# Optimization experiments

Hardware: AMD Instinct MI355X
Metric: run time of the kernel (lower is better)

## Reference

```python
import jax, jax.numpy as jnp
import numpy as np

N = 200000   # 10000 graphs x 20 nodes, stacked
E = 3200000  # avg degree 16
F_IN = 4
H = 32
BN_EPS = 1e-5


def setup_inputs() -> dict:
    key = jax.random.key(0)
    ks = jax.random.split(key, 16)
    s = 0.1
    return {
        "x": jax.random.normal(ks[0], (N, F_IN), jnp.float32),
        "edge_index": jax.random.randint(ks[1], (2, E), 0, N, jnp.int64),
        "edge_weight": jax.random.uniform(ks[2], (E,), jnp.float32),
        "gcn1_w": jax.random.normal(ks[3], (F_IN, H), jnp.float32) * s,
        "gcn1_b": jnp.zeros((H,), jnp.float32),
        "gcn2_w": jax.random.normal(ks[4], (H, H), jnp.float32) * s,
        "gcn2_b": jnp.zeros((H,), jnp.float32),
        "bn1_gamma": jnp.ones((H,), jnp.float32),
        "bn1_beta": jnp.zeros((H,), jnp.float32),
        "bn1_mean": jnp.zeros((H,), jnp.float32),
        "bn1_var": jnp.ones((H,), jnp.float32),
        "bn2_gamma": jnp.ones((H,), jnp.float32),
        "bn2_beta": jnp.zeros((H,), jnp.float32),
        "bn2_mean": jnp.zeros((H,), jnp.float32),
        "bn2_var": jnp.ones((H,), jnp.float32),
        "lstm1_wih": jax.random.normal(ks[5], (4 * H, 2 * H), jnp.float32) * s,
        "lstm1_whh": jax.random.normal(ks[6], (4 * H, H), jnp.float32) * s,
        "lstm1_bih": jax.random.normal(ks[7], (4 * H,), jnp.float32) * s,
        "lstm1_bhh": jax.random.normal(ks[8], (4 * H,), jnp.float32) * s,
        "lstm2_wih": jax.random.normal(ks[9], (4 * H, H), jnp.float32) * s,
        "lstm2_whh": jax.random.normal(ks[10], (4 * H, H), jnp.float32) * s,
        "lstm2_bih": jax.random.normal(ks[11], (4 * H,), jnp.float32) * s,
        "lstm2_bhh": jax.random.normal(ks[12], (4 * H,), jnp.float32) * s,
        "lin_w": jax.random.normal(ks[13], (1, 2 * H + F_IN), jnp.float32) * s,
        "lin_b": jnp.zeros((1,), jnp.float32),
    }


def _gcn_conv(x, src, dst, ew, W, b, n):
    # GCNConv: x @ W, add self-loops (weight 1), symmetric normalization, scatter-add at dst.
    xw = x @ W
    loop = jnp.arange(n)
    s = jnp.concatenate([src, loop])
    d = jnp.concatenate([dst, loop])
    w = jnp.concatenate([ew, jnp.ones((n,), ew.dtype)])
    deg = jax.ops.segment_sum(w, d, num_segments=n)
    dinv = jnp.where(deg > 0, jax.lax.rsqrt(deg), 0.0)
    norm = dinv[s] * w * dinv[d]  # [E+N]
    out = jax.ops.segment_sum(norm[:, None] * xw[s], d, num_segments=n)
    return out + b


def _bn_eval(x, gamma, beta, mean, var):
    return (x - mean) * jax.lax.rsqrt(var + BN_EPS) * gamma + beta


def _lstm_step(x, wih, bih, bhh):
    # single timestep, zero initial (h, c): recurrent W_hh term vanishes.
    gates = x @ wih.T + bih + bhh
    i, f, g, o = jnp.split(gates, 4, axis=1)  # torch gate order i,f,g,o
    c = jax.nn.sigmoid(i) * jnp.tanh(g)
    return jax.nn.sigmoid(o) * jnp.tanh(c)


def reference(x, edge_index, edge_weight, gcn1_w, gcn1_b, gcn2_w, gcn2_b,
              bn1_gamma, bn1_beta, bn1_mean, bn1_var,
              bn2_gamma, bn2_beta, bn2_mean, bn2_var,
              lstm1_wih, lstm1_whh, lstm1_bih, lstm1_bhh,
              lstm2_wih, lstm2_whh, lstm2_bih, lstm2_bhh,
              lin_w, lin_b):
    n = x.shape[0]
    src, dst = edge_index[0], edge_index[1]
    # MPNNLSTM (window=1, eval mode: dropout=identity, BN uses running stats)
    h1 = _bn_eval(jax.nn.relu(_gcn_conv(x, src, dst, edge_weight, gcn1_w, gcn1_b, n)),
                  bn1_gamma, bn1_beta, bn1_mean, bn1_var)
    h2 = _bn_eval(jax.nn.relu(_gcn_conv(h1, src, dst, edge_weight, gcn2_w, gcn2_b, n)),
                  bn2_gamma, bn2_beta, bn2_mean, bn2_var)
    skip = jnp.concatenate([h1, h2], axis=1)  # [N, 2H]
    H1 = _lstm_step(skip, lstm1_wih, lstm1_bih, lstm1_bhh)  # [N, H]
    H2 = _lstm_step(H1, lstm2_wih, lstm2_bih, lstm2_bhh)    # [N, H]
    h = jnp.concatenate([H1, H2, x], axis=1)  # [N, 2H + F_IN]
    # RecurrentGCN head: relu + linear -> [N, 1]
    return jax.nn.relu(h) @ lin_w.T + lin_b
```

## Files before the change

### kernel.cpp

```cpp
#include <hip/hip_runtime.h>
#include <hip/hip_fp16.h>
#include <math.h>

#define BN_EPS 1e-5f
#define HF 32
#define BS 256
#define KEDGE 4096
#define MAXNB 800
#define WQ14 16383.0f
#define WQ22 4194303.0f

typedef _Float16 half8 __attribute__((ext_vector_type(8)));
typedef float f32x4 __attribute__((ext_vector_type(4)));
typedef float f32x2 __attribute__((ext_vector_type(2)));

__device__ __forceinline__ float fsig(float x) {
    return __builtin_amdgcn_rcpf(1.0f + __expf(-x));
}
__device__ __forceinline__ float ftanh(float x) {
    return 1.0f - 2.0f * __builtin_amdgcn_rcpf(1.0f + __expf(2.0f * x));
}


__device__ __forceinline__ float e4m3_to_f32_sw(unsigned v) {
    unsigned s = v & 0x80u, E = (v >> 3) & 0xFu, m = v & 7u;
    float r = E ? ldexpf((float)(8 + m), (int)E - 10) : ldexpf((float)m, -9);
    return s ? -r : r;
}

__device__ __forceinline__ unsigned f32_to_e4m3_sw(float x) {
    float ax = fabsf(x);
    unsigned s = x < 0.0f ? 0x80u : 0u;
    if (!(ax > 0.0f)) return s;
    if (ax >= 448.0f) return s | 0x7Eu;
    int e;
    float m = frexpf(ax, &e);
    int E = e - 1 + 7;
    if (E >= 1) {
        int q = (int)(m * 16.0f + 0.5f);
        if (q == 16) { q = 8; E += 1; if (E > 15) return s | 0x7Eu; }
        return s | (unsigned)(E << 3) | (unsigned)(q - 8);
    }
    int q = (int)(ax * 512.0f + 0.5f);
    if (q > 7) return s | 0x08u;
    return s | (unsigned)q;
}

__device__ __forceinline__ void dec8(uint2 r, float* f) {
#if __has_builtin(__builtin_amdgcn_cvt_pk_f32_fp8)
    f32x2 p0 = __builtin_amdgcn_cvt_pk_f32_fp8((int)r.x, false);
    f32x2 p1 = __builtin_amdgcn_cvt_pk_f32_fp8((int)r.x, true);
    f32x2 p2 = __builtin_amdgcn_cvt_pk_f32_fp8((int)r.y, false);
    f32x2 p3 = __builtin_amdgcn_cvt_pk_f32_fp8((int)r.y, true);
    f[0] = p0[0]; f[1] = p0[1]; f[2] = p1[0]; f[3] = p1[1];
    f[4] = p2[0]; f[5] = p2[1]; f[6] = p3[0]; f[7] = p3[1];
#else
#pragma unroll
    for (int k = 0; k < 4; ++k) f[k] = e4m3_to_f32_sw((r.x >> (8 * k)) & 0xFFu);
#pragma unroll
    for (int k = 0; k < 4; ++k) f[4 + k] = e4m3_to_f32_sw((r.y >> (8 * k)) & 0xFFu);
#endif
}

__device__ __forceinline__ uint2 enc8(const float* o) {
#if __has_builtin(__builtin_amdgcn_cvt_pk_fp8_f32)
    int w0 = 0, w1 = 0;
    w0 = __builtin_amdgcn_cvt_pk_fp8_f32(o[0], o[1], w0, false);
    w0 = __builtin_amdgcn_cvt_pk_fp8_f32(o[2], o[3], w0, true);
    w1 = __builtin_amdgcn_cvt_pk_fp8_f32(o[4], o[5], w1, false);
    w1 = __builtin_amdgcn_cvt_pk_fp8_f32(o[6], o[7], w1, true);
    return make_uint2((unsigned)w0, (unsigned)w1);
#else
    unsigned a = 0, b = 0;
#pragma unroll
    for (int k = 0; k < 4; ++k) a |= f32_to_e4m3_sw(o[k]) << (8 * k);
#pragma unroll
    for (int k = 0; k < 4; ++k) b |= f32_to_e4m3_sw(o[4 + k]) << (8 * k);
    return make_uint2(a, b);
#endif
}


__global__ __launch_bounds__(512) void k_binsort(
        const int* __restrict__ src, const int* __restrict__ dst,
        const float* __restrict__ ew, int E, int NB, int bcap,
        int* __restrict__ gcur, uint2* __restrict__ recs) {
    __shared__ int hist[MAXNB], curs[MAXNB];

    int tid = threadIdx.x;
    int base = blockIdx.x * KEDGE;
    int cnt = min(KEDGE, E - base);

    for (int i = tid; i < NB; i += 512) hist[i] = 0;
    __syncthreads();

    uint2 rec[KEDGE / 512];
#pragma unroll
    for (int k = 0; k < KEDGE / 512; ++k) {
        int i = tid + k * 512;
        if (i < cnt) {
            int s = src[base + i];
            int d = dst[base + i];
            float w = ew[base + i];
            unsigned q = (unsigned)(w * WQ22 + 0.5f);
            if (q > 4194303u) q = 4194303u;
            int b = d >> 8;
            rec[k] = make_uint2(((unsigned)s << 8) | (unsigned)(d & 255),
                                ((unsigned)b << 22) | q);
            atomicAdd(&hist[b], 1);
        }
    }
    __syncthreads();

    for (int b = tid; b < NB; b += 512) {
        int len = hist[b];
        curs[b] = len ? atomicAdd(&gcur[b], len) : 0;
    }
    __syncthreads();

#pragma unroll
    for (int k = 0; k < KEDGE / 512; ++k) {
        int i = tid + k * 512;
        if (i < cnt) {
            uint2 u = rec[k];
            int b = u.y >> 22;
            int off = atomicAdd(&curs[b], 1);
            if (off < bcap) recs[(size_t)b * bcap + off] = u;
        }
    }
}


__global__ __launch_bounds__(512) void k_sortb(
        const uint2* __restrict__ recs, const int* __restrict__ gcur,
        int bcap, int bcap4,
        const float* __restrict__ x, const float* __restrict__ W1,
        unsigned* __restrict__ recs4, int* __restrict__ pstart,
        int* __restrict__ pcnt, float* __restrict__ dinv,
        unsigned char* __restrict__ y18, int n) {
    __shared__ int hist[BS], excl4[BS], curs[BS], wsm[BS];
    __shared__ float sdv[BS];
    __shared__ float sW1[128];

    int b = blockIdx.x, tid = threadIdx.x;
    int cnt = min(gcur[b], bcap);
    const uint2* r = recs + (size_t)b * bcap;
    const float dq = 1.0f / WQ22;

    if (tid < BS) { hist[tid] = 0; wsm[tid] = 0; }
    if (tid >= 256 && tid < 384) sW1[tid - 256] = W1[tid - 256];
    __syncthreads();

    for (int i = tid; i < cnt; i += 512) {
        uint2 u = r[i];
        int dl = u.x & 255;
        atomicAdd(&hist[dl], 1);
        atomicAdd(&wsm[dl], (int)(u.y & 4194303u));
    }
    __syncthreads();

    if (tid < BS) {
        int g = b * BS + tid;
        sdv[tid] = (g < n) ? rsqrtf(1.0f + (float)wsm[tid] * dq) : 0.0f;
    }
    if (tid < 64) {
        int run = 0;
        for (int c = 0; c < BS; c += 64) {
            int idx = c + tid;
            int v = (hist[idx] + 3) & ~3;
            int incl = v;
#pragma unroll
            for (int o = 1; o < 64; o <<= 1) {
                int up = __shfl_up(incl, o, 64);
                if (tid >= o) incl += up;
            }
            int e = run + incl - v;
            excl4[idx] = e; curs[idx] = e;
            run += __shfl(incl, 63, 64);
        }
    }
    __syncthreads();

    unsigned* out4 = recs4 + (size_t)b * bcap4;
    for (int i = tid; i < cnt; i += 512) {
        uint2 u = r[i];
        int dl = u.x & 255;
        int pos = atomicAdd(&curs[dl], 1);
        float qn = (float)(u.y & 4194303u) * dq * sdv[dl];
        unsigned q = (unsigned)(qn * WQ14 + 0.5f);
        if (q > 16383u) q = 16383u;
        out4[pos] = ((u.x >> 8) << 14) | q;
    }

    {
        int node = tid >> 1, half = tid & 1;
        int g = b * BS + node;
        if (g < n) {
            float4 xv = *(const float4*)(x + (size_t)g * 4);
            float sc = sdv[node];
            int f0 = half * 16;
            float o[16];
#pragma unroll
            for (int k = 0; k < 16; ++k)
                o[k] = sc * (xv.x * sW1[f0 + k] + xv.y * sW1[32 + f0 + k] +
                             xv.z * sW1[64 + f0 + k] + xv.w * sW1[96 + f0 + k]);
            uint2 lo = enc8(o), hi = enc8(o + 8);
            *(uint4*)(y18 + ((size_t)g << 5) + half * 16) = make_uint4(lo.x, lo.y, hi.x, hi.y);
        }
    }

    if (tid < BS) {
        int g = b * BS + tid;
        if (g < n) {
            pstart[g] = b * bcap4 + excl4[tid];
            pcnt[g] = hist[tid];
            dinv[g] = sdv[tid];
        }
    }
}


__global__ __launch_bounds__(256) void k_prep(
        const float* __restrict__ wih1, const float* __restrict__ bih1,
        const float* __restrict__ bhh1, const float* __restrict__ wih2,
        const float* __restrict__ bih2, const float* __restrict__ bhh2,
        __half* __restrict__ wp1, __half* __restrict__ wp2,
        float* __restrict__ bsum1, float* __restrict__ bsum2,
        int* __restrict__ gcur, int NB) {
    const int tg[6] = {0, 16, 64, 80, 96, 112};
    int idx = blockIdx.x * 256 + threadIdx.x;
    if (idx < 6144) {
        int t = idx >> 10, rem = idx & 1023;
        int kc = rem >> 9, rem2 = rem & 511;
        int lane = rem2 >> 3, j = rem2 & 7;
        int g = tg[t] + (lane & 15);
        int k = kc * 32 + (lane >> 4) * 8 + j;
        wp1[idx] = __float2half(wih1[g * 64 + k]);
    } else if (idx < 9216) {
        int i2 = idx - 6144;
        int t = i2 >> 9, rem2 = i2 & 511;
        int lane = rem2 >> 3, j = rem2 & 7;
        int g = tg[t] + (lane & 15);
        int k = (lane >> 4) * 8 + j;
        wp2[i2] = __float2half(wih2[g * 32 + k]);
    } else if (idx < 9344) {
        int i = idx - 9216;
        bsum1[i] = bih1[i] + bhh1[i];
    } else if (idx < 9472) {
        int i = idx - 9344;
        bsum2[i] = bih2[i] + bhh2[i];
    } else if (idx < 9472 + NB) {
        gcur[idx - 9472] = 0;
    }
}


__global__ __launch_bounds__(256) void k_g1w2(
        const unsigned* __restrict__ recs4, const int* __restrict__ pstart,
        const int* __restrict__ pcnt, const float* __restrict__ dinv,
        const unsigned char* __restrict__ y18, const float* __restrict__ W2,
        const float* __restrict__ bias, const float* __restrict__ gamma,
        const float* __restrict__ beta, const float* __restrict__ mean,
        const float* __restrict__ var,
        __half* __restrict__ skiph, unsigned char* __restrict__ A8, int n) {
    __shared__ float sW2[1024];
    __shared__ float sh1[64][33];
    int tid = threadIdx.x;
    for (int i = tid; i < 1024; i += 256) sW2[i] = W2[i];
    __syncthreads();

    int nl = tid >> 2;
    int g = blockIdx.x * 64 + nl;
    int lane = tid & 3;
    int fq = lane * 8;
    bool act = g < n;

    float acc[8];
#pragma unroll
    for (int k = 0; k < 8; ++k) acc[k] = 0.0f;

    float dig = 0.0f;
    if (act) {
        dig = dinv[g];
        {
            uint2 sr = ((const uint2*)(y18 + ((size_t)g << 5)))[lane];
            float f[8];
            dec8(sr, f);
#pragma unroll
            for (int k = 0; k < 8; ++k) acc[k] = dig * f[k];
        }

        const float qs = 1.0f / WQ14;
        int cn = pcnt[g];
        const unsigned* r = recs4 + pstart[g];
        int e = 0;
        for (; e + 8 <= cn; e += 8) {
            uint4 ua = *(const uint4*)(r + e);
            uint4 ub = *(const uint4*)(r + e + 4);
            unsigned u[8] = {ua.x, ua.y, ua.z, ua.w, ub.x, ub.y, ub.z, ub.w};
            uint2 rw[8];
#pragma unroll
            for (int q = 0; q < 8; ++q)
                rw[q] = ((const uint2*)(y18 + ((size_t)(u[q] >> 14) << 5)))[lane];
            float nm[8];
#pragma unroll
            for (int q = 0; q < 8; ++q)
                nm[q] = (float)(u[q] & 16383u) * qs;
#pragma unroll
            for (int q = 0; q < 8; ++q) {
                float f[8];
                dec8(rw[q], f);
#pragma unroll
                for (int k = 0; k < 8; ++k) acc[k] += nm[q] * f[k];
            }
        }
        for (; e < cn; ++e) {
            unsigned u0 = r[e];
            uint2 r0 = ((const uint2*)(y18 + ((size_t)(u0 >> 14) << 5)))[lane];
            float n0 = (float)(u0 & 16383u) * qs;
            float f[8];
            dec8(r0, f);
#pragma unroll
            for (int k = 0; k < 8; ++k) acc[k] += n0 * f[k];
        }
    }

    float o[8];
#pragma unroll
    for (int k = 0; k < 8; ++k) {
        float v = fmaxf(acc[k] + bias[fq + k], 0.0f);
        o[k] = (v - mean[fq + k]) * gamma[fq + k] * rsqrtf(var[fq + k] + BN_EPS) + beta[fq + k];
        sh1[nl][fq + k] = o[k];
    }
    if (act) {
        union { __half h[8]; uint4 q; } hv;
#pragma unroll
        for (int k = 0; k < 8; ++k) hv.h[k] = __float2half(o[k]);
        *(uint4*)(skiph + (size_t)g * 64 + fq) = hv.q;
    }
    __syncthreads();

    if (act) {
        float a2[8];
#pragma unroll
        for (int j = 0; j < 8; ++j) a2[j] = 0.0f;
#pragma unroll 4
        for (int k = 0; k < 32; ++k) {
            float h = sh1[nl][k];
            const float* wr = sW2 + k * 32 + fq;
#pragma unroll
            for (int j = 0; j < 8; ++j) a2[j] += h * wr[j];
        }
#pragma unroll
        for (int j = 0; j < 8; ++j) a2[j] *= dig;
        ((uint2*)(A8 + ((size_t)g << 5)))[lane] = enc8(a2);
    }
}


__global__ __launch_bounds__(256) void k_gather8(
        const unsigned* __restrict__ recs4, const int* __restrict__ pstart,
        const int* __restrict__ pcnt, const float* __restrict__ dinv,
        const unsigned char* __restrict__ A8,
        const float* __restrict__ bias, const float* __restrict__ gamma,
        const float* __restrict__ beta, const float* __restrict__ mean,
        const float* __restrict__ var,
        __half* __restrict__ skiph, int uoff, int n) {
    int g = blockIdx.x * 64 + (threadIdx.x >> 2);
    int lane = threadIdx.x & 3;
    if (g >= n) return;

    float dig = dinv[g];
    float acc[8];
    {
        uint2 sr = ((const uint2*)(A8 + ((size_t)g << 5)))[lane];
        float f[8];
        dec8(sr, f);
#pragma unroll
        for (int k = 0; k < 8; ++k) acc[k] = dig * f[k];
    }

    const float qs = 1.0f / WQ14;
    int cn = pcnt[g];
    const unsigned* r = recs4 + pstart[g];
    int e = 0;
    for (; e + 8 <= cn; e += 8) {
        uint4 ua = *(const uint4*)(r + e);
        uint4 ub = *(const uint4*)(r + e + 4);
        unsigned u[8] = {ua.x, ua.y, ua.z, ua.w, ub.x, ub.y, ub.z, ub.w};
        uint2 rw[8];
#pragma unroll
        for (int q = 0; q < 8; ++q)
            rw[q] = ((const uint2*)(A8 + ((size_t)(u[q] >> 14) << 5)))[lane];
        float nm[8];
#pragma unroll
        for (int q = 0; q < 8; ++q)
            nm[q] = (float)(u[q] & 16383u) * qs;
#pragma unroll
        for (int q = 0; q < 8; ++q) {
            float f[8];
            dec8(rw[q], f);
#pragma unroll
            for (int k = 0; k < 8; ++k) acc[k] += nm[q] * f[k];
        }
    }
    for (; e < cn; ++e) {
        unsigned u0 = r[e];
        uint2 r0 = ((const uint2*)(A8 + ((size_t)(u0 >> 14) << 5)))[lane];
        float n0 = (float)(u0 & 16383u) * qs;
        float f0[8];
        dec8(r0, f0);
#pragma unroll
        for (int k = 0; k < 8; ++k) acc[k] += n0 * f0[k];
    }

    int fq = lane * 8;
    union { __half h[8]; uint4 q; } hv;
#pragma unroll
    for (int k = 0; k < 8; ++k) {
        float v = fmaxf(acc[k] + bias[fq + k], 0.0f);
        hv.h[k] = __float2half((v - mean[fq + k]) * gamma[fq + k] * rsqrtf(var[fq + k] + BN_EPS) + beta[fq + k]);
    }
    *(uint4*)(skiph + (size_t)g * 64 + uoff + fq) = hv.q;
}


__global__ __launch_bounds__(256) void k_headm(
        const __half* __restrict__ skiph, const float* __restrict__ x,
        const __half* __restrict__ wp1, const __half* __restrict__ wp2,
        const float* __restrict__ bsum1, const float* __restrict__ bsum2,
        const float* __restrict__ lw, const float* __restrict__ lb,
        float* __restrict__ out, int n) {
    __shared__ __align__(16) __half H1lds[4 * 16 * 40];
    int tid = threadIdx.x;
    int w = tid >> 6, l = tid & 63;
    int quad = l >> 4, c = l & 15;
    int node_base = blockIdx.x * 64 + w * 16;

    int arow = node_base + c; if (arow > n - 1) arow = n - 1;
    const half8* ap = (const half8*)(skiph + (size_t)arow * 64);
    half8 a0 = ap[quad];
    half8 a1 = ap[4 + quad];

    const half8* b1 = (const half8*)wp1;
    f32x4 d[6];
#pragma unroll
    for (int t = 0; t < 6; ++t) {
        f32x4 acc = {0.0f, 0.0f, 0.0f, 0.0f};
        acc = __builtin_amdgcn_mfma_f32_16x16x32_f16(a0, b1[(t * 2 + 0) * 64 + l], acc, 0, 0, 0);
        acc = __builtin_amdgcn_mfma_f32_16x16x32_f16(a1, b1[(t * 2 + 1) * 64 + l], acc, 0, 0, 0);
        d[t] = acc;
    }

    float bi0 = bsum1[c],      bi1 = bsum1[16 + c];
    float bg0 = bsum1[64 + c], bg1 = bsum1[80 + c];
    float bo0 = bsum1[96 + c], bo1 = bsum1[112 + c];
    float lwc0 = lw[c], lwc1 = lw[c + 16];

    float pa[4];
#pragma unroll
    for (int r = 0; r < 4; ++r) {
        float cc0 = fsig(d[0][r] + bi0) * ftanh(d[2][r] + bg0);
        float h0 = fsig(d[4][r] + bo0) * ftanh(cc0);
        float cc1 = fsig(d[1][r] + bi1) * ftanh(d[3][r] + bg1);
        float h1 = fsig(d[5][r] + bo1) * ftanh(cc1);
        pa[r] = fmaxf(h0, 0.0f) * lwc0 + fmaxf(h1, 0.0f) * lwc1;
        __half* hp = H1lds + (w * 16 + quad * 4 + r) * 40;
        hp[c] = __float2half(h0);
        hp[c + 16] = __float2half(h1);
    }
    __syncthreads();

    half8 a2 = *(const half8*)(H1lds + (w * 16 + c) * 40 + quad * 8);

    const half8* b2 = (const half8*)wp2;
    f32x4 e[6];
#pragma unroll
    for (int t = 0; t < 6; ++t) {
        f32x4 acc = {0.0f, 0.0f, 0.0f, 0.0f};
        e[t] = __builtin_amdgcn_mfma_f32_16x16x32_f16(a2, b2[t * 64 + l], acc, 0, 0, 0);
    }

    float ci0 = bsum2[c],      ci1 = bsum2[16 + c];
    float cg0 = bsum2[64 + c], cg1 = bsum2[80 + c];
    float co0 = bsum2[96 + c], co1 = bsum2[112 + c];
    float lw2c0 = lw[32 + c], lw2c1 = lw[48 + c];
#pragma unroll
    for (int r = 0; r < 4; ++r) {
        float cc0 = fsig(e[0][r] + ci0) * ftanh(e[2][r] + cg0);
        float h0 = fsig(e[4][r] + co0) * ftanh(cc0);
        float cc1 = fsig(e[1][r] + ci1) * ftanh(e[3][r] + cg1);
        float h1 = fsig(e[5][r] + co1) * ftanh(cc1);
        pa[r] += fmaxf(h0, 0.0f) * lw2c0 + fmaxf(h1, 0.0f) * lw2c1;
    }

#pragma unroll
    for (int m = 1; m < 16; m <<= 1) {
#pragma unroll
        for (int r = 0; r < 4; ++r) pa[r] += __shfl_xor(pa[r], m, 64);
    }

    if (c < 4) {
        int node = node_base + quad * 4 + c;
        if (node < n) {
            const float4 xv = *(const float4*)(x + (size_t)node * 4);
            out[node] = pa[c] + lb[0]
                + fmaxf(xv.x, 0.0f) * lw[64] + fmaxf(xv.y, 0.0f) * lw[65]
                + fmaxf(xv.z, 0.0f) * lw[66] + fmaxf(xv.w, 0.0f) * lw[67];
        }
    }
}


__global__ void k_initdeg(float* __restrict__ deg, int n) {
    int i = blockIdx.x * blockDim.x + threadIdx.x;
    if (i < n) deg[i] = 1.0f;
}

__global__ void k_deg_only(const int* __restrict__ dst, const float* __restrict__ ew,
                           float* __restrict__ deg, int E) {
    int e = blockIdx.x * blockDim.x + threadIdx.x;
    if (e < E) atomicAdd(&deg[dst[e]], ew[e]);
}

__global__ void k_dinv_f(float* __restrict__ deg, int n) {
    int i = blockIdx.x * blockDim.x + threadIdx.x;
    if (i < n) {
        float d = deg[i];
        deg[i] = d > 0.0f ? rsqrtf(d) : 0.0f;
    }
}

__global__ void k_xw1_f(const float* __restrict__ x, const float* __restrict__ W,
                        float* __restrict__ out, int n) {
    int idx = blockIdx.x * blockDim.x + threadIdx.x;
    if (idx >= n * HF) return;
    int nn = idx >> 5, f = idx & 31;
    const float4 xr = *(const float4*)(x + (size_t)nn * 4);
    out[idx] = xr.x * W[f] + xr.y * W[32 + f] + xr.z * W[64 + f] + xr.w * W[96 + f];
}

__global__ void k_xw2_f(const float* __restrict__ Hin, const float* __restrict__ W,
                        float* __restrict__ out, int n) {
    __shared__ float sW[32 * 32];
    __shared__ float sH[8][32];
    int tid = threadIdx.x;
    for (int i = tid; i < 1024; i += 256) sW[i] = W[i];
    int r = tid >> 5, f = tid & 31;
    int nn = blockIdx.x * 8 + r;
    if (nn < n) sH[r][f] = Hin[(size_t)nn * HF + f];
    __syncthreads();
    if (nn >= n) return;
    float acc = 0.0f;
#pragma unroll
    for (int k = 0; k < 32; ++k) acc += sH[r][k] * sW[k * 32 + f];
    out[(size_t)nn * HF + f] = acc;
}

__global__ void k_selfloop(const float* __restrict__ A, const float* __restrict__ dinv,
                           float* __restrict__ B, int n) {
    int idx = blockIdx.x * blockDim.x + threadIdx.x;
    if (idx >= n * HF) return;
    int nn = idx >> 5;
    float di = dinv[nn];
    B[idx] = di * di * A[idx];
}

__global__ void k_scatter(const int* __restrict__ src, const int* __restrict__ dst,
                          const float* __restrict__ ew, const float* __restrict__ dinv,
                          const float* __restrict__ A, float* __restrict__ B, int total) {
    int idx = blockIdx.x * blockDim.x + threadIdx.x;
    if (idx >= total) return;
    int e = idx >> 5, f = idx & 31;
    int s = src[e], d = dst[e];
    float norm = dinv[s] * ew[e] * dinv[d];
    atomicAdd(&B[d * HF + f], norm * A[s * HF + f]);
}

__global__ void k_post(const float* __restrict__ B, const float* __restrict__ bias,
                       const float* __restrict__ gamma, const float* __restrict__ beta,
                       const float* __restrict__ mean, const float* __restrict__ var,
                       float* __restrict__ Hout, int n) {
    int idx = blockIdx.x * blockDim.x + threadIdx.x;
    if (idx >= n * HF) return;
    int f = idx & 31;
    float v = fmaxf(B[idx] + bias[f], 0.0f);
    float sc = gamma[f] * rsqrtf(var[f] + BN_EPS);
    Hout[idx] = (v - mean[f]) * sc + beta[f];
}

__global__ __launch_bounds__(256) void k_head(
        const float* __restrict__ h1, const float* __restrict__ h2,
        const float* __restrict__ x,
        const float* __restrict__ wih1, const float* __restrict__ bih1, const float* __restrict__ bhh1,
        const float* __restrict__ wih2, const float* __restrict__ bih2, const float* __restrict__ bhh2,
        const float* __restrict__ lw, const float* __restrict__ lb,
        float* __restrict__ out, int n) {
    __shared__ float sH1[32 * 256];
    int tid = threadIdx.x;
    int nn = blockIdx.x * 256 + tid;
    if (nn >= n) return;

    const float4* a = (const float4*)(h1 + (size_t)nn * HF);
    const float4* b = (const float4*)(h2 + (size_t)nn * HF);
    float skip[64];
#pragma unroll
    for (int q = 0; q < 8; ++q) {
        float4 v = a[q];
        skip[4 * q] = v.x; skip[4 * q + 1] = v.y; skip[4 * q + 2] = v.z; skip[4 * q + 3] = v.w;
        float4 u = b[q];
        skip[32 + 4 * q] = u.x; skip[33 + 4 * q] = u.y; skip[34 + 4 * q] = u.z; skip[35 + 4 * q] = u.w;
    }

    float oa = lb[0];
#pragma unroll 1
    for (int j = 0; j < 32; ++j) {
        const float4* wi = (const float4*)(wih1 + (size_t)j * 64);
        const float4* wg = (const float4*)(wih1 + (size_t)(64 + j) * 64);
        const float4* wo = (const float4*)(wih1 + (size_t)(96 + j) * 64);
        float gi = bih1[j] + bhh1[j];
        float gg = bih1[64 + j] + bhh1[64 + j];
        float go = bih1[96 + j] + bhh1[96 + j];
#pragma unroll
        for (int q = 0; q < 16; ++q) {
            float4 aa = wi[q], bb = wg[q], cc4 = wo[q];
            float s0 = skip[4 * q], s1 = skip[4 * q + 1], s2 = skip[4 * q + 2], s3 = skip[4 * q + 3];
            gi += aa.x * s0 + aa.y * s1 + aa.z * s2 + aa.w * s3;
            gg += bb.x * s0 + bb.y * s1 + bb.z * s2 + bb.w * s3;
            go += cc4.x * s0 + cc4.y * s1 + cc4.z * s2 + cc4.w * s3;
        }
        float cc = fsig(gi) * ftanh(gg);
        float hh = fsig(go) * ftanh(cc);
        sH1[j * 256 + tid] = hh;
        oa += fmaxf(hh, 0.0f) * lw[j];
    }

#pragma unroll 1
    for (int j = 0; j < 32; ++j) {
        const float4* wi = (const float4*)(wih2 + (size_t)j * 32);
        const float4* wg = (const float4*)(wih2 + (size_t)(64 + j) * 32);
        const float4* wo = (const float4*)(wih2 + (size_t)(96 + j) * 32);
        float gi = bih2[j] + bhh2[j];
        float gg = bih2[64 + j] + bhh2[64 + j];
        float go = bih2[96 + j] + bhh2[96 + j];
#pragma unroll
        for (int q = 0; q < 8; ++q) {
            float4 aa = wi[q], bb = wg[q], cc4 = wo[q];
            float s0 = sH1[(4 * q) * 256 + tid], s1 = sH1[(4 * q + 1) * 256 + tid];
            float s2 = sH1[(4 * q + 2) * 256 + tid], s3 = sH1[(4 * q + 3) * 256 + tid];
            gi += aa.x * s0 + aa.y * s1 + aa.z * s2 + aa.w * s3;
            gg += bb.x * s0 + bb.y * s1 + bb.z * s2 + bb.w * s3;
            go += cc4.x * s0 + cc4.y * s1 + cc4.z * s2 + cc4.w * s3;
        }
        float cc = fsig(gi) * ftanh(gg);
        float hh = fsig(go) * ftanh(cc);
        oa += fmaxf(hh, 0.0f) * lw[32 + j];
    }

    const float4 xv = *(const float4*)(x + (size_t)nn * 4);
    oa += fmaxf(xv.x, 0.0f) * lw[64] + fmaxf(xv.y, 0.0f) * lw[65] +
          fmaxf(xv.z, 0.0f) * lw[66] + fmaxf(xv.w, 0.0f) * lw[67];
    out[nn] = oa;
}


extern "C" void kernel_launch(void* const* d_in, const int* in_sizes, int n_in,
                              void* d_out, int out_size, void* d_ws, size_t ws_size,
                              hipStream_t stream) {
    const float* x   = (const float*)d_in[0];
    const int*   ei  = (const int*)d_in[1];
    const float* ew  = (const float*)d_in[2];
    const float* g1w = (const float*)d_in[3];
    const float* g1b = (const float*)d_in[4];
    const float* g2w = (const float*)d_in[5];
    const float* g2b = (const float*)d_in[6];
    const float* bn1g = (const float*)d_in[7];
    const float* bn1b = (const float*)d_in[8];
    const float* bn1m = (const float*)d_in[9];
    const float* bn1v = (const float*)d_in[10];
    const float* bn2g = (const float*)d_in[11];
    const float* bn2b = (const float*)d_in[12];
    const float* bn2m = (const float*)d_in[13];
    const float* bn2v = (const float*)d_in[14];
    const float* w1ih = (const float*)d_in[15];
    const float* b1ih = (const float*)d_in[17];
    const float* b1hh = (const float*)d_in[18];
    const float* w2ih = (const float*)d_in[19];
    const float* b2ih = (const float*)d_in[21];
    const float* b2hh = (const float*)d_in[22];
    const float* lw   = (const float*)d_in[23];
    const float* lb   = (const float*)d_in[24];
    float* out = (float*)d_out;

    const int N = in_sizes[0] / 4;
    const int E = in_sizes[2];
    const int* src = ei;
    const int* dst = ei + E;

    const int T = 256;
    const int NB = (N + BS - 1) / BS;
    long long meanb = ((long long)BS * E) / (N > 0 ? N : 1);
    int bcap = (int)(meanb + meanb / 4 + 128);
    bcap = (bcap + 3) & ~3;
    int bcap4 = bcap + 3 * BS;

    char* p = (char*)d_ws;
    auto alloc = [&](size_t bytes) { char* q = p; p += (bytes + 255) & ~(size_t)255; return q; };
    int*      gcur   = (int*)alloc(sizeof(int) * NB);
    uint2*    recs   = (uint2*)alloc(sizeof(uint2) * (size_t)NB * bcap);
    unsigned* recs4  = (unsigned*)alloc(sizeof(unsigned) * (size_t)NB * bcap4);
    float*    dinv   = (float*)alloc(sizeof(float) * N);
    int*      pstart = (int*)alloc(sizeof(int) * N);
    int*      pcnt   = (int*)alloc(sizeof(int) * N);
    unsigned char* y18 = (unsigned char*)alloc((size_t)N * HF);
    unsigned char* A8  = (unsigned char*)alloc((size_t)N * HF);
    __half*   skiph  = (__half*)alloc(sizeof(__half) * (size_t)N * 64);
    __half*   wp1    = (__half*)alloc(sizeof(__half) * 6144);
    __half*   wp2    = (__half*)alloc(sizeof(__half) * 3072);
    float*    bsum1  = (float*)alloc(sizeof(float) * 128);
    float*    bsum2  = (float*)alloc(sizeof(float) * 128);
    size_t need = (size_t)(p - (char*)d_ws);

    int bN  = (N + T - 1) / T;
    int bE  = (E + T - 1) / T;
    int bNF = (N * HF + T - 1) / T;
    int bN8 = (N + 7) / 8;
    int bG  = (N + 63) / 64;
    int bBin = (E + KEDGE - 1) / KEDGE;
    int bPrep = (9472 + NB + 255) / 256;

    if (ws_size >= need && NB <= MAXNB && N <= (1 << 18)) {
        k_prep<<<bPrep, 256, 0, stream>>>(w1ih, b1ih, b1hh, w2ih, b2ih, b2hh,
                                          wp1, wp2, bsum1, bsum2, gcur, NB);
        k_binsort<<<bBin, 512, 0, stream>>>(src, dst, ew, E, NB, bcap, gcur, recs);
        k_sortb<<<NB, 512, 0, stream>>>(recs, gcur, bcap, bcap4, x, g1w,
                                        recs4, pstart, pcnt, dinv, y18, N);

        k_g1w2<<<bG, T, 0, stream>>>(recs4, pstart, pcnt, dinv, y18, g2w,
                                     g1b, bn1g, bn1b, bn1m, bn1v, skiph, A8, N);
        k_gather8<<<bG, T, 0, stream>>>(recs4, pstart, pcnt, dinv, A8,
                                        g2b, bn2g, bn2b, bn2m, bn2v, skiph, 32, N);
        k_headm<<<bG, T, 0, stream>>>(skiph, x, wp1, wp2, bsum1, bsum2,
                                      lw, lb, out, N);
    } else {
        size_t Npad = ((size_t)N + 255) & ~(size_t)255;
        float* fdinv = (float*)d_ws;
        float* fA = fdinv + Npad;
        float* fB = fA + (size_t)N * HF;
        float* fC = fB + (size_t)N * HF;
        int bEF = (int)(((long long)E * HF + T - 1) / T);
        int bH = (N + 255) / 256;

        k_initdeg<<<bN, T, 0, stream>>>(fdinv, N);
        k_deg_only<<<bE, T, 0, stream>>>(dst, ew, fdinv, E);
        k_dinv_f<<<bN, T, 0, stream>>>(fdinv, N);

        k_xw1_f<<<bNF, T, 0, stream>>>(x, g1w, fA, N);
        k_selfloop<<<bNF, T, 0, stream>>>(fA, fdinv, fB, N);
        k_scatter<<<bEF, T, 0, stream>>>(src, dst, ew, fdinv, fA, fB, E * HF);
        k_post<<<bNF, T, 0, stream>>>(fB, g1b, bn1g, bn1b, bn1m, bn1v, fC, N);

        k_xw2_f<<<bN8, T, 0, stream>>>(fC, g2w, fA, N);
        k_selfloop<<<bNF, T, 0, stream>>>(fA, fdinv, fB, N);
        k_scatter<<<bEF, T, 0, stream>>>(src, dst, ew, fdinv, fA, fB, E * HF);
        k_post<<<bNF, T, 0, stream>>>(fB, g2b, bn2g, bn2b, bn2m, bn2v, fB, N);

        k_head<<<bH, T, 0, stream>>>(fC, fB, x, w1ih, b1ih, b1hh, w2ih, b2ih, b2hh,
                                     lw, lb, out, N);
    }
}
```

Before: 296.9 us.

## Fuse second GCN gather into LSTM head, vectorize binsort loads, prefetch edge records

The second GCN aggregation kernel is merged into the LSTM/linear head kernel. The h2 features now stay in shared memory instead of going through global memory, so skiph shrinks to only h1 (32 halves per node). Binsort now has each thread load 8 contiguous edges with 128-bit vector loads instead of strided scalar loads. The gather loops software-prefetch the next 8 edge records. The fused kernel uses more shared memory and registers, which may lower occupancy for the latency-bound gather.

```diff
diff --git a/kernel.cpp b/kernel.cpp
--- a/kernel.cpp
+++ b/kernel.cpp
@@ -94,20 +94,42 @@
     for (int i = tid; i < NB; i += 512) hist[i] = 0;
     __syncthreads();
 
-    uint2 rec[KEDGE / 512];
-#pragma unroll
-    for (int k = 0; k < KEDGE / 512; ++k) {
-        int i = tid + k * 512;
-        if (i < cnt) {
-            int s = src[base + i];
-            int d = dst[base + i];
-            float w = ew[base + i];
-            unsigned q = (unsigned)(w * WQ22 + 0.5f);
-            if (q > 4194303u) q = 4194303u;
-            int b = d >> 8;
-            rec[k] = make_uint2(((unsigned)s << 8) | (unsigned)(d & 255),
-                                ((unsigned)b << 22) | q);
-            atomicAdd(&hist[b], 1);
+    uint2 rec[8];
+    int nmine = 0;
+    int eb = base + tid * 8;
+    if (tid * 8 < cnt) {
+        nmine = min(8, cnt - tid * 8);
+        if (nmine == 8) {
+            int4 s0 = *(const int4*)(src + eb);
+            int4 s1 = *(const int4*)(src + eb + 4);
+            int4 d0 = *(const int4*)(dst + eb);
+            int4 d1 = *(const int4*)(dst + eb + 4);
+            float4 w0 = *(const float4*)(ew + eb);
+            float4 w1 = *(const float4*)(ew + eb + 4);
+            int ss[8] = {s0.x, s0.y, s0.z, s0.w, s1.x, s1.y, s1.z, s1.w};
+            int dd[8] = {d0.x, d0.y, d0.z, d0.w, d1.x, d1.y, d1.z, d1.w};
+            float ww[8] = {w0.x, w0.y, w0.z, w0.w, w1.x, w1.y, w1.z, w1.w};
+#pragma unroll
+            for (int k = 0; k < 8; ++k) {
+                unsigned q = (unsigned)(ww[k] * WQ22 + 0.5f);
+                if (q > 4194303u) q = 4194303u;
+                int b = dd[k] >> 8;
+                rec[k] = make_uint2(((unsigned)ss[k] << 8) | (unsigned)(dd[k] & 255),
+                                    ((unsigned)b << 22) | q);
+                atomicAdd(&hist[b], 1);
+            }
+        } else {
+            for (int k = 0; k < nmine; ++k) {
+                int s = src[eb + k];
+                int d = dst[eb + k];
+                float w = ew[eb + k];
+                unsigned q = (unsigned)(w * WQ22 + 0.5f);
+                if (q > 4194303u) q = 4194303u;
+                int b = d >> 8;
+                rec[k] = make_uint2(((unsigned)s << 8) | (unsigned)(d & 255),
+                                    ((unsigned)b << 22) | q);
+                atomicAdd(&hist[b], 1);
+            }
         }
     }
     __syncthreads();
@@ -118,15 +140,11 @@
     }
     __syncthreads();
 
-#pragma unroll
-    for (int k = 0; k < KEDGE / 512; ++k) {
-        int i = tid + k * 512;
-        if (i < cnt) {
-            uint2 u = rec[k];
-            int b = u.y >> 22;
-            int off = atomicAdd(&curs[b], 1);
-            if (off < bcap) recs[(size_t)b * bcap + off] = u;
-        }
+    for (int k = 0; k < nmine; ++k) {
+        uint2 u = rec[k];
+        int b = u.y >> 22;
+        int off = atomicAdd(&curs[b], 1);
+        if (off < bcap) recs[(size_t)b * bcap + off] = u;
     }
 }
 
@@ -293,10 +311,12 @@
         const float qs = 1.0f / WQ14;
         int cn = pcnt[g];
         const unsigned* r = recs4 + pstart[g];
+        uint4 na, nb;
+        if (8 <= cn) { na = *(const uint4*)(r); nb = *(const uint4*)(r + 4); }
         int e = 0;
         for (; e + 8 <= cn; e += 8) {
-            uint4 ua = *(const uint4*)(r + e);
-            uint4 ub = *(const uint4*)(r + e + 4);
+            uint4 ua = na, ub = nb;
+            if (e + 16 <= cn) { na = *(const uint4*)(r + e + 8); nb = *(const uint4*)(r + e + 12); }
             unsigned u[8] = {ua.x, ua.y, ua.z, ua.w, ub.x, ub.y, ub.z, ub.w};
             uint2 rw[8];
 #pragma unroll
@@ -336,7 +356,7 @@
         union { __half h[8]; uint4 q; } hv;
 #pragma unroll
         for (int k = 0; k < 8; ++k) hv.h[k] = __float2half(o[k]);
-        *(uint4*)(skiph + (size_t)g * 64 + fq) = hv.q;
+        *(uint4*)(skiph + (size_t)g * 32 + fq) = hv.q;
     }
     __syncthreads();
 
@@ -358,98 +378,105 @@
 }
 
 
-__global__ __launch_bounds__(256) void k_gather8(
+__global__ __launch_bounds__(256) void k_g2head(
         const unsigned* __restrict__ recs4, const int* __restrict__ pstart,
         const int* __restrict__ pcnt, const float* __restrict__ dinv,
         const unsigned char* __restrict__ A8,
         const float* __restrict__ bias, const float* __restrict__ gamma,
         const float* __restrict__ beta, const float* __restrict__ mean,
         const float* __restrict__ var,
-        __half* __restrict__ skiph, int uoff, int n) {
-    int g = blockIdx.x * 64 + (threadIdx.x >> 2);
-    int lane = threadIdx.x & 3;
-    if (g >= n) return;
-
-    float dig = dinv[g];
-    float acc[8];
-    {
-        uint2 sr = ((const uint2*)(A8 + ((size_t)g << 5)))[lane];
-        float f[8];
-        dec8(sr, f);
-#pragma unroll
-        for (int k = 0; k < 8; ++k) acc[k] = dig * f[k];
-    }
-
-    const float qs = 1.0f / WQ14;
-    int cn = pcnt[g];
-    const unsigned* r = recs4 + pstart[g];
-    int e = 0;
-    for (; e + 8 <= cn; e += 8) {
-        uint4 ua = *(const uint4*)(r + e);
-        uint4 ub = *(const uint4*)(r + e + 4);
-        unsigned u[8] = {ua.x, ua.y, ua.z, ua.w, ub.x, ub.y, ub.z, ub.w};
-        uint2 rw[8];
-#pragma unroll
-        for (int q = 0; q < 8; ++q)
-            rw[q] = ((const uint2*)(A8 + ((size_t)(u[q] >> 14) << 5)))[lane];
-        float nm[8];
-#pragma unroll
-        for (int q = 0; q < 8; ++q)
-            nm[q] = (float)(u[q] & 16383u) * qs;
-#pragma unroll
-        for (int q = 0; q < 8; ++q) {
-            float f[8];
-            dec8(rw[q], f);
-#pragma unroll
-            for (int k = 0; k < 8; ++k) acc[k] += nm[q] * f[k];
-        }
-    }
-    for (; e < cn; ++e) {
-        unsigned u0 = r[e];
-        uint2 r0 = ((const uint2*)(A8 + ((size_t)(u0 >> 14) << 5)))[lane];
-        float n0 = (float)(u0 & 16383u) * qs;
-        float f0[8];
-        dec8(r0, f0);
-#pragma unroll
-        for (int k = 0; k < 8; ++k) acc[k] += n0 * f0[k];
-    }
-
-    int fq = lane * 8;
-    union { __half h[8]; uint4 q; } hv;
-#pragma unroll
-    for (int k = 0; k < 8; ++k) {
-        float v = fmaxf(acc[k] + bias[fq + k], 0.0f);
-        hv.h[k] = __float2half((v - mean[fq + k]) * gamma[fq + k] * rsqrtf(var[fq + k] + BN_EPS) + beta[fq + k]);
-    }
-    *(uint4*)(skiph + (size_t)g * 64 + uoff + fq) = hv.q;
-}
-
-
-__global__ __launch_bounds__(256) void k_headm(
         const __half* __restrict__ skiph, const float* __restrict__ x,
         const __half* __restrict__ wp1, const __half* __restrict__ wp2,
         const float* __restrict__ bsum1, const float* __restrict__ bsum2,
         const float* __restrict__ lw, const float* __restrict__ lb,
         float* __restrict__ out, int n) {
+    __shared__ __align__(16) __half h2s[64][40];
     __shared__ __align__(16) __half H1lds[4 * 16 * 40];
     int tid = threadIdx.x;
+    int nl = tid >> 2;
+    int g = blockIdx.x * 64 + nl;
+    int lane = tid & 3;
+    int fq = lane * 8;
+    bool act = g < n;
+
+    float acc[8];
+#pragma unroll
+    for (int k = 0; k < 8; ++k) acc[k] = 0.0f;
+
+    if (act) {
+        float dig = dinv[g];
+        {
+            uint2 sr = ((const uint2*)(A8 + ((size_t)g << 5)))[lane];
+            float f[8];
+            dec8(sr, f);
+#pragma unroll
+            for (int k = 0; k < 8; ++k) acc[k] = dig * f[k];
+        }
+
+        const float qs = 1.0f / WQ14;
+        int cn = pcnt[g];
+        const unsigned* r = recs4 + pstart[g];
+        uint4 na, nb;
+        if (8 <= cn) { na = *(const uint4*)(r); nb = *(const uint4*)(r + 4); }
+        int e = 0;
+        for (; e + 8 <= cn; e += 8) {
+            uint4 ua = na, ub = nb;
+            if (e + 16 <= cn) { na = *(const uint4*)(r + e + 8); nb = *(const uint4*)(r + e + 12); }
+            unsigned u[8] = {ua.x, ua.y, ua.z, ua.w, ub.x, ub.y, ub.z, ub.w};
+            uint2 rw[8];
+#pragma unroll
+            for (int q = 0; q < 8; ++q)
+                rw[q] = ((const uint2*)(A8 + ((size_t)(u[q] >> 14) << 5)))[lane];
+            float nm[8];
+#pragma unroll
+            for (int q = 0; q < 8; ++q)
+                nm[q] = (float)(u[q] & 16383u) * qs;
+#pragma unroll
+            for (int q = 0; q < 8; ++q) {
+                float f[8];
+                dec8(rw[q], f);
+#pragma unroll
+                for (int k = 0; k < 8; ++k) acc[k] += nm[q] * f[k];
+            }
+        }
+        for (; e < cn; ++e) {
+            unsigned u0 = r[e];
+            uint2 r0 = ((const uint2*)(A8 + ((size_t)(u0 >> 14) << 5)))[lane];
+            float n0 = (float)(u0 & 16383u) * qs;
+            float f0[8];
+            dec8(r0, f0);
+#pragma unroll
+            for (int k = 0; k < 8; ++k) acc[k] += n0 * f0[k];
+        }
+
+        union { __half h[8]; uint4 q; } hv;
+#pragma unroll
+        for (int k = 0; k < 8; ++k) {
+            float v = fmaxf(acc[k] + bias[fq + k], 0.0f);
+            hv.h[k] = __float2half((v - mean[fq + k]) * gamma[fq + k] *
+                                   rsqrtf(var[fq + k] + BN_EPS) + beta[fq + k]);
+        }
+        *(uint4*)(&h2s[nl][fq]) = hv.q;
+    }
+    __syncthreads();
+
     int w = tid >> 6, l = tid & 63;
     int quad = l >> 4, c = l & 15;
     int node_base = blockIdx.x * 64 + w * 16;
 
     int arow = node_base + c; if (arow > n - 1) arow = n - 1;
-    const half8* ap = (const half8*)(skiph + (size_t)arow * 64);
-    half8 a0 = ap[quad];
-    half8 a1 = ap[4 + quad];
+    int lr = arow - blockIdx.x * 64;
+    half8 a0 = *(const half8*)(skiph + (size_t)arow * 32 + quad * 8);
+    half8 a1 = *(const half8*)(&h2s[lr][quad * 8]);
 
     const half8* b1 = (const half8*)wp1;
     f32x4 d[6];
 #pragma unroll
     for (int t = 0; t < 6; ++t) {
-        f32x4 acc = {0.0f, 0.0f, 0.0f, 0.0f};
-        acc = __builtin_amdgcn_mfma_f32_16x16x32_f16(a0, b1[(t * 2 + 0) * 64 + l], acc, 0, 0, 0);
-        acc = __builtin_amdgcn_mfma_f32_16x16x32_f16(a1, b1[(t * 2 + 1) * 64 + l], acc, 0, 0, 0);
-        d[t] = acc;
+        f32x4 ac = {0.0f, 0.0f, 0.0f, 0.0f};
+        ac = __builtin_amdgcn_mfma_f32_16x16x32_f16(a0, b1[(t * 2 + 0) * 64 + l], ac, 0, 0, 0);
+        ac = __builtin_amdgcn_mfma_f32_16x16x32_f16(a1, b1[(t * 2 + 1) * 64 + l], ac, 0, 0, 0);
+        d[t] = ac;
     }
 
     float bi0 = bsum1[c],      bi1 = bsum1[16 + c];
@@ -474,11 +501,11 @@
     half8 a2 = *(const half8*)(H1lds + (w * 16 + c) * 40 + quad * 8);
 
     const half8* b2 = (const half8*)wp2;
-    f32x4 e[6];
+    f32x4 e2[6];
 #pragma unroll
     for (int t = 0; t < 6; ++t) {
-        f32x4 acc = {0.0f, 0.0f, 0.0f, 0.0f};
-        e[t] = __builtin_amdgcn_mfma_f32_16x16x32_f16(a2, b2[t * 64 + l], acc, 0, 0, 0);
+        f32x4 ac = {0.0f, 0.0f, 0.0f, 0.0f};
+        e2[t] = __builtin_amdgcn_mfma_f32_16x16x32_f16(a2, b2[t * 64 + l], ac, 0, 0, 0);
     }
 
     float ci0 = bsum2[c],      ci1 = bsum2[16 + c];
@@ -487,10 +514,10 @@
     float lw2c0 = lw[32 + c], lw2c1 = lw[48 + c];
 #pragma unroll
     for (int r = 0; r < 4; ++r) {
-        float cc0 = fsig(e[0][r] + ci0) * ftanh(e[2][r] + cg0);
-        float h0 = fsig(e[4][r] + co0) * ftanh(cc0);
-        float cc1 = fsig(e[1][r] + ci1) * ftanh(e[3][r] + cg1);
-        float h1 = fsig(e[5][r] + co1) * ftanh(cc1);
+        float cc0 = fsig(e2[0][r] + ci0) * ftanh(e2[2][r] + cg0);
+        float h0 = fsig(e2[4][r] + co0) * ftanh(cc0);
+        float cc1 = fsig(e2[1][r] + ci1) * ftanh(e2[3][r] + cg1);
+        float h1 = fsig(e2[5][r] + co1) * ftanh(cc1);
         pa[r] += fmaxf(h0, 0.0f) * lw2c0 + fmaxf(h1, 0.0f) * lw2c1;
     }
 
@@ -714,7 +741,7 @@
     int*      pcnt   = (int*)alloc(sizeof(int) * N);
     unsigned char* y18 = (unsigned char*)alloc((size_t)N * HF);
     unsigned char* A8  = (unsigned char*)alloc((size_t)N * HF);
-    __half*   skiph  = (__half*)alloc(sizeof(__half) * (size_t)N * 64);
+    __half*   skiph  = (__half*)alloc(sizeof(__half) * (size_t)N * 32);
     __half*   wp1    = (__half*)alloc(sizeof(__half) * 6144);
     __half*   wp2    = (__half*)alloc(sizeof(__half) * 3072);
     float*    bsum1  = (float*)alloc(sizeof(float) * 128);
@@ -738,10 +765,10 @@
 
         k_g1w2<<<bG, T, 0, stream>>>(recs4, pstart, pcnt, dinv, y18, g2w,
                                      g1b, bn1g, bn1b, bn1m, bn1v, skiph, A8, N);
-        k_gather8<<<bG, T, 0, stream>>>(recs4, pstart, pcnt, dinv, A8,
-                                        g2b, bn2g, bn2b, bn2m, bn2v, skiph, 32, N);
-        k_headm<<<bG, T, 0, stream>>>(skiph, x, wp1, wp2, bsum1, bsum2,
-                                      lw, lb, out, N);
+        k_g2head<<<bG, T, 0, stream>>>(recs4, pstart, pcnt, dinv, A8,
+                                       g2b, bn2g, bn2b, bn2m, bn2v,
+                                       skiph, x, wp1, wp2, bsum1, bsum2,
+                                       lw, lb, out, N);
     } else {
         size_t Npad = ((size_t)N + 255) & ~(size_t)255;
         float* fdinv = (float*)d_ws;
```

Measured after the change: 293.7 us. Within noise of the previous version (-1.1%).
